# Optimization experiments

Hardware: AMD Instinct MI355X
Metric: run time of the kernel (lower is better)

The kernel has to match this reference:

```python
import jax, jax.numpy as jnp
import numpy as np
from jax import lax

IC = 256
NK = [512, 256, 128]
PS = 16.0  # patch_size
EPS = 1e-5


def conv3x3(x, w, b):
    y = lax.conv_general_dilated(x, w, (1, 1), ((1, 1), (1, 1)),
                                 dimension_numbers=('NCHW', 'OIHW', 'NCHW'))
    return y + b[None, :, None, None]


def conv1x1(x, w, b):
    y = lax.conv_general_dilated(x, w, (1, 1), ((0, 0), (0, 0)),
                                 dimension_numbers=('NCHW', 'OIHW', 'NCHW'))
    return y + b[None, :, None, None]


def bn_eval(x, g, b, m, v):
    inv = lax.rsqrt(v + EPS)
    return (x - m[None, :, None, None]) * (g * inv)[None, :, None, None] + b[None, :, None, None]


def tower(x, w, b, g, bb, m, v, lvl):
    # conv3x3 -> per-level BN (ModuleListDial) -> ReLU, depth=1
    return jax.nn.relu(bn_eval(conv3x3(x, w, b), g[lvl], bb[lvl], m[lvl], v[lvl]))


def setup_inputs() -> dict:
    key = jax.random.key(0)
    ks = jax.random.split(key, 32)
    d = {
        'feat0': jax.random.normal(ks[0], (4, IC, 128, 128), jnp.float32),
        'feat1': jax.random.normal(ks[1], (4, IC, 64, 64), jnp.float32),
        'feat2': jax.random.normal(ks[2], (4, IC, 32, 32), jnp.float32),
        'target_coords': jax.random.randint(ks[3], (2, 32, 32), 0, 32, jnp.int32),
    }
    ki = 4
    for p in ['share', 'ent', 'pat']:
        d[p + '_w'] = jax.random.normal(ks[ki], (IC, IC, 3, 3), jnp.float32) * 0.02; ki += 1
        d[p + '_b'] = jnp.zeros((IC,), jnp.float32)
        d[p + '_g'] = jnp.ones((3, IC), jnp.float32)
        d[p + '_bb'] = jnp.zeros((3, IC), jnp.float32)
        d[p + '_m'] = jax.random.normal(ks[ki], (3, IC), jnp.float32) * 0.1; ki += 1
        d[p + '_v'] = jax.random.uniform(ks[ki], (3, IC), jnp.float32, 0.5, 1.5); ki += 1
    d['ehead_w'] = jax.random.normal(ks[ki], (1, IC, 1, 1), jnp.float32) * 0.05; ki += 1
    d['ehead_b'] = jnp.zeros((1,), jnp.float32)
    d['head_w'] = jax.random.normal(ks[ki], (4, IC), jnp.float32) * 0.05; ki += 1
    d['head_b'] = jnp.zeros((4,), jnp.float32)
    return d


def reference(feat0, feat1, feat2, target_coords,
              share_w, share_b, share_g, share_bb, share_m, share_v,
              ent_w, ent_b, ent_g, ent_bb, ent_m, ent_v,
              pat_w, pat_b, pat_g, pat_bb, pat_m, pat_v,
              ehead_w, ehead_b, head_w, head_b):
    coords = target_coords  # [2, h', w'] (row, col)
    cflat = coords.reshape(2, -1).T  # [P, 2]
    outs = []
    for lvl, (x, nk) in enumerate(zip([feat0, feat1, feat2], NK)):
        xs = tower(x, share_w, share_b, share_g, share_bb, share_m, share_v, lvl)
        ex = tower(xs, ent_w, ent_b, ent_g, ent_bb, ent_m, ent_v, lvl)
        em = jax.nn.sigmoid(conv1x1(ex, ehead_w, ehead_b))  # [B,1,H,W]
        B, C, H, W = ex.shape
        # entropy at candidate anchor points -> [B, P]
        ape = em[:, 0, coords[0], coords[1]].reshape(B, -1)
        _, top_idx = lax.top_k(ape, nk)  # [B, nk]
        xy = cflat[top_idx]  # [B, nk, 2]
        lin = xy[..., 0] * W + xy[..., 1]  # linear index into HW
        px = tower(xs, pat_w, pat_b, pat_g, pat_bb, pat_m, pat_v, lvl)
        pxf = px.reshape(B, C, H * W).transpose(0, 2, 1)  # [B, HW, C]
        af = jnp.take_along_axis(pxf, lin[..., None], axis=1)  # [B, nk, C]
        pc = jax.nn.sigmoid(af @ head_w.T + head_b)  # [B, nk, 4]
        ax = xy[..., 0].astype(pc.dtype)
        ay = xy[..., 1].astype(pc.dtype)
        final = jnp.stack([ax - PS * pc[..., 0], ay - PS * pc[..., 1],
                           ax + PS * pc[..., 2], ay + PS * pc[..., 3]], axis=-1)
        outs += [em, final, xy]
    return tuple(outs)
```

## Files before the change

kernel.cpp:

```cpp
#include <hip/hip_runtime.h>
#include <cstdint>
#include <cstddef>


typedef _Float16 f16;
typedef _Float16 f16x4 __attribute__((ext_vector_type(4)));
typedef _Float16 f16x8 __attribute__((ext_vector_type(8)));
typedef float    f32x4 __attribute__((ext_vector_type(4)));

constexpr int C_CH = 256;
constexpr int KTOT = 2304;
constexpr int PAT_POS = 3584;
constexpr int PAT_N   = PAT_POS * C_CH;

#define GLL16(g, l) __builtin_amdgcn_global_load_lds(                        \
    (const __attribute__((address_space(1))) unsigned int*)(g),              \
    (__attribute__((address_space(3))) unsigned int*)(l), 16, 0, 0)

__global__ __launch_bounds__(256)
void prep_weights_kernel(const float* __restrict__ sw, const float* __restrict__ ew,
                         const float* __restrict__ pw,
                         f16* __restrict__ wTs, f16* __restrict__ wTe,
                         f16* __restrict__ wTsL, f16* __restrict__ wTeL,
                         f16* __restrict__ wTp, f16* __restrict__ wTpL, int n)
{
    int i = blockIdx.x * 256 + threadIdx.x;
    if (i >= n) return;
    const int oc = i / KTOT;
    const int kp = i - oc * KTOT;
    const int tap = kp >> 8;
    const int ic  = kp & 255;
    const int src = oc * KTOT + ic * 9 + tap;
    const float vs = sw[src];
    const f16 hs = (f16)vs;
    wTs[i]  = hs;
    wTsL[i] = (f16)((vs - (float)hs) * 1024.f);
    const float ve = ew[src];
    const f16 he = (f16)ve;
    wTe[i]  = he;
    wTeL[i] = (f16)((ve - (float)he) * 1024.f);
    const float vp = pw[src];
    const f16 hp = (f16)vp;
    wTp[i]  = hp;
    wTpL[i] = (f16)((vp - (float)hp) * 1024.f);
}

__global__ __launch_bounds__(256)
void prep_bn_kernel(const float* sg, const float* sbb, const float* smm,
                    const float* svv, const float* sb,
                    const float* eg, const float* ebb, const float* emm,
                    const float* evv, const float* eb,
                    float* __restrict__ scale, float* __restrict__ shift)
{
    int i = blockIdx.x * 256 + threadIdx.x;
    if (i >= 1536) return;
    const int tw = i / 768;
    const int r  = i - tw * 768;
    const int oc = r & 255;
    float g, bbv, m, v, cb;
    if (tw == 0) { g = sg[r]; bbv = sbb[r]; m = smm[r]; v = svv[r]; cb = sb[oc]; }
    else         { g = eg[r]; bbv = ebb[r]; m = emm[r]; v = evv[r]; cb = eb[oc]; }
    const float inv = 1.0f / sqrtf(v + 1e-5f);
    const float sc = g * inv;
    scale[i] = sc;
    shift[i] = (cb - m) * sc + bbv;
}

__global__ __launch_bounds__(256)
void zero16_kernel(f16x8* __restrict__ p, int n8)
{
    const int i = blockIdx.x * 256 + threadIdx.x;
    if (i < n8) p[i] = (f16x8){};
}

__global__ __launch_bounds__(256)
void fpad16_fill_kernel(const float* __restrict__ feat0,
                        const float* __restrict__ feat1,
                        const float* __restrict__ feat2,
                        f16* __restrict__ xH, f16* __restrict__ xL)
{
    const int h    = blockIdx.x;
    const int lvlb = blockIdx.y;
    const int lvl  = lvlb >> 2, b = lvlb & 3;
    const int logW = 7 - lvl, H = 128 >> lvl;
    if (h >= H) return;
    const int Wv = (H >= 34) ? 34 : 32;
    const int tid = threadIdx.x;
    const float* f = (lvl == 0) ? feat0 : (lvl == 1 ? feat1 : feat2);

    __shared__ float T[34][257];

    const int wl = tid & 31;
    const int cg = tid >> 5;
#pragma unroll
    for (int cb = 0; cb < 32; cb++) {
        const int c = cb * 8 + cg;
        const float* row = f + (((size_t)(b * C_CH + c)) << (2 * logW))
                             + ((size_t)h << logW);
        T[wl][c] = row[wl];
        if (wl < 2 && (wl + 32) < Wv) T[wl + 32][c] = row[wl + 32];
    }
    __syncthreads();
    const size_t rb = ((size_t)lvlb * 1296 + (size_t)(h + 2) * 36 + 2) * 256 + tid;
    for (int w = 0; w < Wv; w++) {
        const float v = T[w][tid];
        const f16 hh = (f16)v;
        xH[rb + (size_t)w * 256] = hh;
        xL[rb + (size_t)w * 256] = (f16)((v - (float)hh) * 1024.f);
    }
}

__global__ __launch_bounds__(256)
void pad_hwc_kernel(const float* __restrict__ feat, f16* __restrict__ xT,
                    int H, int logW)
{
    const int W = 1 << logW;
    const int HW = H << logW;
    const int WP = W + 2, HP = H + 2;
    const int tid = threadIdx.x;
    const int nt  = HW >> 6;
    const int b   = blockIdx.x / nt;
    const int p0  = (blockIdx.x - b * nt) * 64;

    __shared__ f16 T[64][264];

    const int cBase = tid >> 4;
    const int pl4   = (tid & 15) * 4;
#pragma unroll
    for (int it = 0; it < 16; it++) {
        const int c = it * 16 + cBase;
        const float4 v = *(const float4*)(feat + (size_t)(b * C_CH + c) * HW + p0 + pl4);
        T[pl4 + 0][c] = (f16)v.x;
        T[pl4 + 1][c] = (f16)v.y;
        T[pl4 + 2][c] = (f16)v.z;
        T[pl4 + 3][c] = (f16)v.w;
    }
    __syncthreads();
    const int pl = tid >> 2;
    const int c0 = (tid & 3) * 64;
    const int p  = p0 + pl;
    const int h  = p >> logW, w = p & (W - 1);
    f16* dst = xT + ((size_t)(b * HP + h + 1) * WP + (w + 1)) * C_CH + c0;
#pragma unroll
    for (int i = 0; i < 64; i += 8)
        *(f16x8*)(dst + i) = *(const f16x8*)&T[pl][c0 + i];
}

__global__ __launch_bounds__(256)
void zero_cl_border_kernel(f16* __restrict__ xT, int H, int W, int n)
{
    const int WP = W + 2, HP = H + 2;
    const int BS = 2 * WP + 2 * H;
    int i = blockIdx.x * 256 + threadIdx.x;
    if (i >= n) return;
    const int ch = (i & 7) * 32;
    const int bc = i >> 3;
    const int b  = bc / BS;
    const int e  = bc - b * BS;
    int padpos;
    if (e < WP)            padpos = e;
    else if (e < 2 * WP)   padpos = (H + 1) * WP + (e - WP);
    else {
        const int e2 = e - 2 * WP;
        padpos = ((e2 >> 1) + 1) * WP + ((e2 & 1) ? (W + 1) : 0);
    }
    f16* dst = xT + ((size_t)b * HP * WP + padpos) * C_CH + ch;
    const f16x8 z = {};
#pragma unroll
    for (int j = 0; j < 32; j += 8) *(f16x8*)(dst + j) = z;
}

__global__ __launch_bounds__(256, 3)
void conv_mfma_kernel(const f16* __restrict__ xT, const f16* __restrict__ wT,
                      const float* __restrict__ scale,
                      const float* __restrict__ shift,
                      f16* __restrict__ y, int H, int logW, int opad)
{
    const int W  = 1 << logW;
    const int WP = W + 2, HP = H + 2;
    const int HW = H << logW;
    const int tid  = threadIdx.x;
    const int wv   = tid >> 6, lane = tid & 63;

    const int nwg = gridDim.x;
    const int bid = blockIdx.x;
    const int wg  = (bid & 7) * (nwg >> 3) + (bid >> 3);
    const int ocBase = (wg & 1) * 128;
    const int pBase  = (wg >> 1) * 128;
    const int b    = pBase / HW;
    const int rem0 = pBase - b * HW;

    __shared__ f16 sbuf[16384];

    f32x4 acc[4][4];
#pragma unroll
    for (int i = 0; i < 4; i++)
#pragma unroll
        for (int j = 0; j < 4; j++) acc[i][j] = (f32x4){0.f, 0.f, 0.f, 0.f};

    const int lr = lane >> 2, ls = lane & 3;
    const int r0 = (wv * 2) * 16 + lr;
    const int r1 = (wv * 2 + 1) * 16 + lr;
    const int c0s = (ls ^ ((r0 >> 1) & 3)) * 8;
    const int c1s = (ls ^ ((r1 >> 1) & 3)) * 8;
    const f16* aSrc0 = wT + (size_t)(ocBase + r0) * KTOT + c0s;
    const f16* aSrc1 = wT + (size_t)(ocBase + r1) * KTOT + c1s;
    const int pp0 = rem0 + r0, pp1 = rem0 + r1;
    const f16* bSrc0 = xT + ((size_t)(b * HP + (pp0 >> logW) + 1) * WP
                             + (pp0 & (W - 1)) + 1) * C_CH + c0s;
    const f16* bSrc1 = xT + ((size_t)(b * HP + (pp1 >> logW) + 1) * WP
                             + (pp1 & (W - 1)) + 1) * C_CH + c1s;

    const int rw = (wv & 1) * 64;
    const int cw = (wv >> 1) * 64;
    const int lm = lane & 15, lq = lane >> 4;
    int aOff[4], bOff[4];
#pragma unroll
    for (int mi = 0; mi < 4; mi++) {
        const int R = rw + mi * 16 + lm;
        aOff[mi] = R * 32 + ((lq ^ ((R >> 1) & 3)) << 3);
    }
#pragma unroll
    for (int ni = 0; ni < 4; ni++) {
        const int R = cw + ni * 16 + lm;
        bOff[ni] = 4096 + R * 32 + ((lq ^ ((R >> 1) & 3)) << 3);
    }

    auto STAGE = [&](int kn, int nb) {
        const int tap = kn >> 8;
        const int kh  = tap / 3;
        const int kw  = tap - 3 * kh;
        const int tOff = ((kh - 1) * WP + (kw - 1)) * C_CH + (kn & 255);
        f16* lb = &sbuf[nb * 8192 + wv * 1024];
        GLL16(aSrc0 + kn, lb);
        GLL16(aSrc1 + kn, lb + 512);
        GLL16(bSrc0 + tOff, lb + 4096);
        GLL16(bSrc1 + tOff, lb + 4096 + 512);
    };

    STAGE(0, 0);
    __syncthreads();
    int cur = 0;
    for (int k0 = 0; k0 < KTOT; k0 += 32) {
        if (k0 + 32 < KTOT) STAGE(k0 + 32, cur ^ 1);
        const f16* sb = &sbuf[cur * 8192];
        f16x8 af[4], bf[4];
#pragma unroll
        for (int mi = 0; mi < 4; mi++) af[mi] = *(const f16x8*)(sb + aOff[mi]);
#pragma unroll
        for (int ni = 0; ni < 4; ni++) bf[ni] = *(const f16x8*)(sb + bOff[ni]);
#pragma unroll
        for (int mi = 0; mi < 4; mi++)
#pragma unroll
            for (int ni = 0; ni < 4; ni++)
                acc[mi][ni] = __builtin_amdgcn_mfma_f32_16x16x32_f16(
                    af[mi], bf[ni], acc[mi][ni], 0, 0, 0);
        __syncthreads();
        cur ^= 1;
    }

    float sc[4][4], sh[4][4];
#pragma unroll
    for (int mi = 0; mi < 4; mi++)
#pragma unroll
        for (int r = 0; r < 4; r++) {
            const int oc = ocBase + rw + mi * 16 + lq * 4 + r;
            sc[mi][r] = scale[oc];
            sh[mi][r] = shift[oc];
        }
#pragma unroll
    for (int ni = 0; ni < 4; ni++) {
        const int pp = rem0 + cw + ni * 16 + lm;
        size_t dst;
        if (opad) {
            const int h2 = pp >> logW, w2 = pp & (W - 1);
            dst = ((size_t)(b * HP + h2 + 1) * WP + (w2 + 1)) * C_CH;
        } else {
            dst = (size_t)(pBase + cw + ni * 16 + lm) * C_CH;
        }
#pragma unroll
        for (int mi = 0; mi < 4; mi++) {
            const int ocb = ocBase + rw + mi * 16 + lq * 4;
            f16x4 o;
#pragma unroll
            for (int r = 0; r < 4; r++)
                o[r] = (f16)fmaxf(fmaf(acc[mi][ni][r], sc[mi][r], sh[mi][r]), 0.f);
            *(f16x4*)(y + dst + ocb) = o;
        }
    }
}

__global__ __launch_bounds__(256)
void ehead_em_f16_kernel(const f16* __restrict__ ex, const float* __restrict__ ehw,
                         const float* __restrict__ ehb, float* __restrict__ em)
{
    const int wv   = threadIdx.x >> 6;
    const int lane = threadIdx.x & 63;
    const int posBase = (blockIdx.x * 4 + wv) * 8;
    const int sp = lane >> 3;
    const int t  = lane & 7;
    const int cg = t * 32;
    const f16* base = ex + (size_t)(posBase + sp) * C_CH + cg;
    float s = 0.f;
#pragma unroll
    for (int i = 0; i < 32; i += 8) {
        const f16x8 v = *(const f16x8*)(base + i);
#pragma unroll
        for (int j = 0; j < 8; j++)
            s = fmaf((float)v[j], ehw[cg + i + j], s);
    }
    s += __shfl_xor(s, 1);
    s += __shfl_xor(s, 2);
    s += __shfl_xor(s, 4);
    if (t == 0) em[posBase + sp] = 1.0f / (1.0f + expf(-(s + ehb[0])));
}

template<bool IS_SHARE>
__global__ __launch_bounds__(256, 2)
void exact_full_kernel(const f16* __restrict__ xHg, const f16* __restrict__ xLg,
                       const f16* __restrict__ wH, const f16* __restrict__ wL,
                       const float* __restrict__ scale,
                       const float* __restrict__ shift,
                       float* __restrict__ xsp,
                       f16* __restrict__ xOH, f16* __restrict__ xOL,
                       float* __restrict__ apePart, const float* __restrict__ ehw)
{
    constexpr int NTL    = IS_SHARE ? 19 : 16;
    constexpr int IPITCH = IS_SHARE ? 36 : 34;
    constexpr int IPLANE = IS_SHARE ? 1296 : 1156;

    const int tid  = threadIdx.x;
    const int wv   = tid >> 6, lane = tid & 63;

    const int nwg = gridDim.x;
    const int bid = blockIdx.x;
    const int wgs = (bid & 7) * (nwg >> 3) + (bid >> 3);
    const int ocq = wgs & 3;
    const int ti  = wgs >> 2;
    const int lvlb = ti / NTL;
    const int tile = ti - lvlb * NTL;
    const int posBase = tile * 64;
    const int ocBase  = ocq * 64;
    const int lvl  = lvlb >> 2;

    __shared__ f16 sbuf[16384];

    f32x4 accH[2][2], accX[2][2];
#pragma unroll
    for (int i = 0; i < 2; i++)
#pragma unroll
        for (int j = 0; j < 2; j++) {
            accH[i][j] = (f32x4){0.f, 0.f, 0.f, 0.f};
            accX[i][j] = (f32x4){0.f, 0.f, 0.f, 0.f};
        }

    const int lr = lane >> 2, ls = lane & 3;
    const int rA = wv * 16 + lr;
    const int cAs = (ls ^ ((rA >> 1) & 3)) * 8;
    const f16* aSrcH = wH + (size_t)(ocBase + rA) * KTOT + cAs;
    const f16* aSrcL = wL + (size_t)(ocBase + rA) * KTOT + cAs;

    int n = posBase + rA;
    if (IS_SHARE && n > 1155) n = 1155;
    int po;
    if (IS_SHARE) { const int ph = n / 34; po = ph * 36 + (n - ph * 34); }
    else          { po = (n >> 5) * 34 + (n & 31); }
    const f16* bSrcH = xHg + ((size_t)lvlb * IPLANE + po) * 256 + cAs;
    const f16* bSrcL = xLg + ((size_t)lvlb * IPLANE + po) * 256 + cAs;

    const int rw = (wv & 1) * 32;
    const int cw = (wv >> 1) * 32;
    const int lm = lane & 15, lq = lane >> 4;
    int aOff[2], bOff[2];
#pragma unroll
    for (int mi = 0; mi < 2; mi++) {
        const int R = rw + mi * 16 + lm;
        aOff[mi] = R * 32 + ((lq ^ ((R >> 1) & 3)) << 3);
    }
#pragma unroll
    for (int ni = 0; ni < 2; ni++) {
        const int R = cw + ni * 16 + lm;
        bOff[ni] = R * 32 + ((lq ^ ((R >> 1) & 3)) << 3);
    }

    auto STAGE = [&](int kn, int nb) {
        const int tap = kn >> 8;
        const int th  = tap / 3;
        const int tOff = (th * IPITCH + (tap - 3 * th)) * 256 + (kn & 255);
        f16* lb = &sbuf[nb * 8192 + wv * 512];
        GLL16(aSrcH + kn, lb);
        GLL16(aSrcL + kn, lb + 2048);
        GLL16(bSrcH + tOff, lb + 4096);
        GLL16(bSrcL + tOff, lb + 6144);
    };

    STAGE(0, 0);
    __syncthreads();
    int cur = 0;
    for (int ko = 0; ko < KTOT; ko += 32) {
        if (ko + 32 < KTOT) STAGE(ko + 32, cur ^ 1);
        const f16* sb = &sbuf[cur * 8192];
        f16x8 aH[2], aL[2];
#pragma unroll
        for (int mi = 0; mi < 2; mi++) {
            aH[mi] = *(const f16x8*)(sb + aOff[mi]);
            aL[mi] = *(const f16x8*)(sb + 2048 + aOff[mi]);
        }
#pragma unroll
        for (int ni = 0; ni < 2; ni++) {
            const f16x8 bh = *(const f16x8*)(sb + 4096 + bOff[ni]);
            const f16x8 bl = *(const f16x8*)(sb + 6144 + bOff[ni]);
#pragma unroll
            for (int mi = 0; mi < 2; mi++)
                accH[mi][ni] = __builtin_amdgcn_mfma_f32_16x16x32_f16(
                    aH[mi], bh, accH[mi][ni], 0, 0, 0);
#pragma unroll
            for (int mi = 0; mi < 2; mi++)
                accX[mi][ni] = __builtin_amdgcn_mfma_f32_16x16x32_f16(
                    aH[mi], bl, accX[mi][ni], 0, 0, 0);
#pragma unroll
            for (int mi = 0; mi < 2; mi++)
                accX[mi][ni] = __builtin_amdgcn_mfma_f32_16x16x32_f16(
                    aL[mi], bh, accX[mi][ni], 0, 0, 0);
        }
        __syncthreads();
        cur ^= 1;
    }

    if constexpr (IS_SHARE) {
#pragma unroll
        for (int mi = 0; mi < 2; mi++)
#pragma unroll
            for (int r = 0; r < 4; r++) {
                const int chl = rw + mi * 16 + lq * 4 + r;
                const int oc  = ocBase + chl;
                const float sc = scale[lvl * 256 + oc];
                const float sh = shift[lvl * 256 + oc];
#pragma unroll
                for (int ni = 0; ni < 2; ni++) {
                    const int pl  = cw + ni * 16 + lm;
                    const int nn  = posBase + pl;
                    const float val = accH[mi][ni][r]
                                    + accX[mi][ni][r] * (1.0f / 1024.0f);
                    const int ph = nn / 34;
                    const int pw = nn - ph * 34;
                    const bool valid = (nn < 1156) && (ph >= 1) && (pw >= 1) &&
                                       (lvl < 2 || (ph <= 32 && pw <= 32));
                    const float o = valid ? fmaxf(fmaf(val, sc, sh), 0.f) : 0.f;
                    if (nn < 1156)
                        xsp[((size_t)(lvlb * 256 + oc)) * 1156 + nn] = o;
                    const f16 h = (f16)o;
                    sbuf[pl * 72 + chl]        = h;
                    sbuf[4608 + pl * 72 + chl] = (f16)((o - (float)h) * 1024.f);
                }
            }
        __syncthreads();
        const int p  = tid >> 2;
        const int cg = (tid & 3) * 16;
        const int n2 = posBase + p;
        if (n2 < 1156) {
            const size_t gb = ((size_t)lvlb * 1156 + n2) * 256 + ocBase + cg;
            *(f16x8*)(xOH + gb)     = *(const f16x8*)(sbuf + p * 72 + cg);
            *(f16x8*)(xOH + gb + 8) = *(const f16x8*)(sbuf + p * 72 + cg + 8);
            *(f16x8*)(xOL + gb)     = *(const f16x8*)(sbuf + 4608 + p * 72 + cg);
            *(f16x8*)(xOL + gb + 8) = *(const f16x8*)(sbuf + 4608 + p * 72 + cg + 8);
        }
    } else {
        float* pa = (float*)sbuf;
        float pni[2] = {0.f, 0.f};
#pragma unroll
        for (int mi = 0; mi < 2; mi++)
#pragma unroll
            for (int r = 0; r < 4; r++) {
                const int oc = ocBase + rw + mi * 16 + lq * 4 + r;
                const float sc = scale[768 + lvl * 256 + oc];
                const float sh = shift[768 + lvl * 256 + oc];
                const float w  = ehw[oc];
#pragma unroll
                for (int ni = 0; ni < 2; ni++) {
                    const float val = accH[mi][ni][r]
                                    + accX[mi][ni][r] * (1.0f / 1024.0f);
                    pni[ni] = fmaf(w, fmaxf(fmaf(val, sc, sh), 0.f), pni[ni]);
                }
            }
        const int slot = lq + 4 * (wv & 1);
#pragma unroll
        for (int ni = 0; ni < 2; ni++)
            pa[(cw + ni * 16 + lm) * 8 + slot] = pni[ni];
        __syncthreads();
        if (tid < 64) {
            float s = pa[tid * 8];
#pragma unroll
            for (int j = 1; j < 8; j++) s += pa[tid * 8 + j];
            apePart[(size_t)ocq * 12288 + lvlb * 1024 + posBase + tid] = s;
        }
    }
}

__global__ __launch_bounds__(256)
void ape_fin_kernel(const float* __restrict__ apePart,
                    const float* __restrict__ ehb, float* __restrict__ ape)
{
    const int i = blockIdx.x * 256 + threadIdx.x;
    if (i >= 12288) return;
    float s = apePart[i];
    s += apePart[12288 + i];
    s += apePart[24576 + i];
    s += apePart[36864 + i];
    ape[i] = 1.0f / (1.0f + expf(-(s + ehb[0])));
}

__global__ __launch_bounds__(1024)
void topk_all_kernel(const float* __restrict__ ape, const int* __restrict__ coords,
                     int* __restrict__ xy_int, float* __restrict__ out,
                     int xo0, int xo1, int xo2)
{
    const int lvl = blockIdx.x >> 2;
    const int b   = blockIdx.x & 3;
    const int nk  = 512 >> lvl;
    const int tid = threadIdx.x;
    __shared__ unsigned long long keys[1024];

    const int rr = coords[tid] & 31;
    const int cc0 = coords[1024 + tid] & 31;
    const float v = ape[lvl * 4096 + (b << 10) + (rr << 5) + cc0];
    unsigned u = __float_as_uint(v);
    unsigned mono = (u & 0x80000000u) ? ~u : (u | 0x80000000u);
    keys[tid] = (((unsigned long long)(~mono)) << 32) | (unsigned)tid;
    __syncthreads();

    for (int k = 2; k <= 1024; k <<= 1) {
        for (int j = k >> 1; j > 0; j >>= 1) {
            const int ixj = tid ^ j;
            if (ixj > tid) {
                const bool up = ((tid & k) == 0);
                const unsigned long long a = keys[tid], c = keys[ixj];
                if ((a > c) == up) { keys[tid] = c; keys[ixj] = a; }
            }
            __syncthreads();
        }
    }

    if (tid < nk) {
        const int i  = (int)(keys[tid] & 0x3FFu);
        const int r  = coords[i] & 31;
        const int c  = coords[1024 + i] & 31;
        const int intOff = 8192 - (8192 >> lvl);
        const int o  = intOff + (b * nk + tid) * 2;
        xy_int[o]     = r;
        xy_int[o + 1] = c;
        const int xo = (lvl == 0) ? xo0 : (lvl == 1 ? xo1 : xo2);
        out[xo + (b * nk + tid) * 2]     = (float)r;
        out[xo + (b * nk + tid) * 2 + 1] = (float)c;
    }
}

__global__ __launch_bounds__(256, 2)
void pat_mfma_kernel(const f16* __restrict__ xHg, const f16* __restrict__ xLg,
                     const f16* __restrict__ wH, const f16* __restrict__ wL,
                     const int* __restrict__ xy_int,
                     float* __restrict__ part)
{
    const int tid = threadIdx.x;
    const int wv  = tid >> 6, lane = tid & 63;
    const int nwg = gridDim.x;
    const int bid = blockIdx.x;
    const int wgs = (bid & 7) * (nwg >> 3) + (bid >> 3);
    const int z   = wgs & 1;
    const int ocq = (wgs >> 1) & 3;
    const int ti  = wgs >> 3;
    int lvl, pL;
    if (ti < 64)      { lvl = 0; pL = ti * 32; }
    else if (ti < 96) { lvl = 1; pL = (ti - 64) * 32; }
    else              { lvl = 2; pL = (ti - 96) * 32; }
    const int nk   = 512 >> lvl;
    const int bb   = pL / nk;
    const int lvlb = lvl * 4 + bb;
    const int intOff   = 8192 - (8192 >> lvl);
    const int posStart = 4096 - (4096 >> lvl);
    const int ocBase = ocq * 64;
    const int kStart = z * 1152;

    __shared__ f16 sbuf[12288];
    __shared__ int pofs[32];

    if (tid < 32) {
        const int n = pL + tid;
        const int r = xy_int[intOff + n * 2]     & 31;
        const int c = xy_int[intOff + n * 2 + 1] & 31;
        pofs[tid] = r * 34 + c;
    }
    __syncthreads();

    f32x4 accH[2], accX[2];
#pragma unroll
    for (int i = 0; i < 2; i++) {
        accH[i] = (f32x4){0.f, 0.f, 0.f, 0.f};
        accX[i] = (f32x4){0.f, 0.f, 0.f, 0.f};
    }

    const int lr = lane >> 2, ls = lane & 3;
    const int rA  = wv * 16 + lr;
    const int cAs = (ls ^ ((rA >> 1) & 3)) * 8;
    const f16* aSrcH = wH + (size_t)(ocBase + rA) * KTOT + kStart + cAs;
    const f16* aSrcL = wL + (size_t)(ocBase + rA) * KTOT + kStart + cAs;
    const int rB  = (wv & 1) * 16 + lr;
    const int cBs = (ls ^ ((rB >> 1) & 3)) * 8;
    const f16* bBase = (wv < 2) ? xHg : xLg;
    const f16* bSrc = bBase + ((size_t)lvlb * 1156 + pofs[rB]) * 256 + cBs;
    const int bDst = ((wv < 2) ? 4096 : 5120) + (wv & 1) * 512;

    const int rw = (wv & 1) * 32;
    const int pw = (wv >> 1) * 16;
    const int lm = lane & 15, lq = lane >> 4;
    int aOff[2];
#pragma unroll
    for (int mi = 0; mi < 2; mi++) {
        const int R = rw + mi * 16 + lm;
        aOff[mi] = R * 32 + ((lq ^ ((R >> 1) & 3)) << 3);
    }
    const int Rb = pw + lm;
    const int bOff = 4096 + Rb * 32 + ((lq ^ ((Rb >> 1) & 3)) << 3);

    auto STAGE = [&](int kRel, int nb) {
        const int kAbs = kStart + kRel;
        const int tap  = kAbs >> 8;
        const int th   = tap / 3;
        const int tOff = (th * 34 + (tap - 3 * th)) * 256 + (kAbs & 255);
        f16* base = &sbuf[nb * 6144];
        GLL16(aSrcH + kRel, base + wv * 512);
        GLL16(aSrcL + kRel, base + 2048 + wv * 512);
        GLL16(bSrc + tOff,  base + bDst);
    };

    STAGE(0, 0);
    __syncthreads();
    int cur = 0;
    for (int ko = 0; ko < 1152; ko += 32) {
        if (ko + 32 < 1152) STAGE(ko + 32, cur ^ 1);
        const f16* sb = &sbuf[cur * 6144];
        f16x8 aH[2], aL[2];
#pragma unroll
        for (int mi = 0; mi < 2; mi++) {
            aH[mi] = *(const f16x8*)(sb + aOff[mi]);
            aL[mi] = *(const f16x8*)(sb + 2048 + aOff[mi]);
        }
        const f16x8 bh = *(const f16x8*)(sb + bOff);
        const f16x8 bl = *(const f16x8*)(sb + 1024 + bOff);
#pragma unroll
        for (int mi = 0; mi < 2; mi++)
            accH[mi] = __builtin_amdgcn_mfma_f32_16x16x32_f16(
                aH[mi], bh, accH[mi], 0, 0, 0);
#pragma unroll
        for (int mi = 0; mi < 2; mi++)
            accX[mi] = __builtin_amdgcn_mfma_f32_16x16x32_f16(
                aH[mi], bl, accX[mi], 0, 0, 0);
#pragma unroll
        for (int mi = 0; mi < 2; mi++)
            accX[mi] = __builtin_amdgcn_mfma_f32_16x16x32_f16(
                aL[mi], bh, accX[mi], 0, 0, 0);
        __syncthreads();
        cur ^= 1;
    }

    float* op = part + (size_t)z * PAT_N
              + (size_t)(posStart + pL + pw + lm) * C_CH + ocBase;
#pragma unroll
    for (int mi = 0; mi < 2; mi++)
#pragma unroll
        for (int r = 0; r < 4; r++)
            op[rw + mi * 16 + lq * 4 + r] =
                accH[mi][r] + accX[mi][r] * (1.0f / 1024.0f);
}

__global__ __launch_bounds__(256)
void pat_reduce_kernel(const float* __restrict__ part,
                       const float* __restrict__ cb,
                       const float* __restrict__ bng, const float* __restrict__ bnb,
                       const float* __restrict__ bnm, const float* __restrict__ bnv,
                       float* __restrict__ af)
{
    const int i4 = (blockIdx.x * 256 + threadIdx.x) * 4;
    if (i4 >= PAT_N) return;
    const int pos = i4 >> 8;
    const int oc0 = i4 & 255;
    const int lvl = (pos < 2048) ? 0 : (pos < 3072 ? 1 : 2);
    float4 s = *(const float4*)(part + i4);
    {
        const float4 t = *(const float4*)(part + (size_t)PAT_N + i4);
        s.x += t.x; s.y += t.y; s.z += t.z; s.w += t.w;
    }
    const float4 g  = *(const float4*)(bng + lvl * 256 + oc0);
    const float4 bb = *(const float4*)(bnb + lvl * 256 + oc0);
    const float4 m  = *(const float4*)(bnm + lvl * 256 + oc0);
    const float4 v  = *(const float4*)(bnv + lvl * 256 + oc0);
    const float4 cb4 = *(const float4*)(cb + oc0);
    float4 o;
    {
        float inv = 1.0f / sqrtf(v.x + 1e-5f); float sc = g.x * inv;
        o.x = fmaxf(fmaf(s.x, sc, (cb4.x - m.x) * sc + bb.x), 0.f);
        inv = 1.0f / sqrtf(v.y + 1e-5f); sc = g.y * inv;
        o.y = fmaxf(fmaf(s.y, sc, (cb4.y - m.y) * sc + bb.y), 0.f);
        inv = 1.0f / sqrtf(v.z + 1e-5f); sc = g.z * inv;
        o.z = fmaxf(fmaf(s.z, sc, (cb4.z - m.z) * sc + bb.z), 0.f);
        inv = 1.0f / sqrtf(v.w + 1e-5f); sc = g.w * inv;
        o.w = fmaxf(fmaf(s.w, sc, (cb4.w - m.w) * sc + bb.w), 0.f);
    }
    *(float4*)(af + i4) = o;
}

__global__ __launch_bounds__(256)
void head_final_all_kernel(const float* __restrict__ af, const float* __restrict__ hw,
                           const float* __restrict__ hb, const int* __restrict__ xy_int,
                           float* __restrict__ out, int fo0, int fo1, int fo2)
{
    const int pos = blockIdx.x;
    const int lvl = (pos < 2048) ? 0 : (pos < 3072 ? 1 : 2);
    const int local = pos - (4096 - (4096 >> lvl));
    const int intOff = 8192 - (8192 >> lvl);
    const int fo = (lvl == 0) ? fo0 : (lvl == 1 ? fo1 : fo2);
    const int tid  = threadIdx.x;
    const int j4   = tid >> 6;
    const int lane = tid & 63;
    const float* a = af + (size_t)pos * C_CH;
    const float* w = hw + j4 * C_CH;
    float sum = 0.f;
#pragma unroll
    for (int i = 0; i < 4; i++)
        sum = fmaf(a[lane + 64 * i], w[lane + 64 * i], sum);
#pragma unroll
    for (int off = 32; off > 0; off >>= 1) sum += __shfl_down(sum, off);
    if (lane == 0) {
        const float pc = 1.0f / (1.0f + expf(-(sum + hb[j4])));
        const float ax = (float)xy_int[intOff + local * 2];
        const float ay = (float)xy_int[intOff + local * 2 + 1];
        float val;
        if      (j4 == 0) val = ax - 16.0f * pc;
        else if (j4 == 1) val = ay - 16.0f * pc;
        else if (j4 == 2) val = ax + 16.0f * pc;
        else              val = ay + 16.0f * pc;
        out[fo + local * 4 + j4] = val;
    }
}

extern "C" void kernel_launch(void* const* d_in, const int* in_sizes, int n_in,
                              void* d_out, int out_size, void* d_ws, size_t ws_size,
                              hipStream_t stream) {
    const float* feat[3] = {(const float*)d_in[0], (const float*)d_in[1],
                            (const float*)d_in[2]};
    const int*   coords  = (const int*)d_in[3];
    const float* sw  = (const float*)d_in[4];
    const float* sb  = (const float*)d_in[5];
    const float* sg  = (const float*)d_in[6];
    const float* sbb = (const float*)d_in[7];
    const float* smm = (const float*)d_in[8];
    const float* svv = (const float*)d_in[9];
    const float* ew  = (const float*)d_in[10];
    const float* eb  = (const float*)d_in[11];
    const float* eg  = (const float*)d_in[12];
    const float* ebb = (const float*)d_in[13];
    const float* emm = (const float*)d_in[14];
    const float* evv = (const float*)d_in[15];
    const float* pw  = (const float*)d_in[16];
    const float* pb  = (const float*)d_in[17];
    const float* pg  = (const float*)d_in[18];
    const float* pbb = (const float*)d_in[19];
    const float* pmm = (const float*)d_in[20];
    const float* pvv = (const float*)d_in[21];
    const float* ehw = (const float*)d_in[22];
    const float* ehb = (const float*)d_in[23];
    const float* hww = (const float*)d_in[24];
    const float* hbb = (const float*)d_in[25];

    float* out = (float*)d_out;
    char*  ws  = (char*)d_ws;

    f16*   wTs    = (f16*)(ws);
    f16*   wTe    = (f16*)(ws + 1310720);
    f16*   wTsL   = (f16*)(ws + 2621440);
    f16*   wTeL   = (f16*)(ws + 3932160);
    float* scales = (float*)(ws + 5242880);
    float* shifts = (float*)(ws + 5251072);
    f16*   fpadH  = (f16*)(ws + 6291456);
    f16*   fpadL  = (f16*)(ws + 14254080);
    float* patPart= (float*)(ws + 6291456);
    float* af     = (float*)(ws + 23068672);
    f16*   wTp    = (f16*)(ws + 27262976);
    f16*   wTpL   = (f16*)(ws + 28573696);
    f16*   xspH   = (f16*)(ws + 90177536);
    f16*   xspL   = (f16*)(ws + 97280000);
    float* xsp    = (float*)(ws + 104857600);
    float* ape    = (float*)(ws + 119537664);
    int*   xy_int = (int*)  (ws + 119603200);
    float* apePart= (float*)(ws + 119668736);
    f16*   featT  = (f16*)(ws + 27262976);
    f16*   xsT    = (f16*)(ws + 65011712);
    f16*   exT    = (f16*)(ws + 27262976);

    const int Hs[3]    = {128, 64, 32};
    const int logWs[3] = {7, 6, 5};
    const int nks[3]   = {512, 256, 128};

    size_t off = 0;
    size_t emOff[3], finOff[3], xyOff[3];
    for (int l = 0; l < 3; l++) {
        const int HW = Hs[l] * Hs[l];
        emOff[l]  = off; off += (size_t)4 * HW;
        finOff[l] = off; off += (size_t)4 * nks[l] * 4;
        xyOff[l]  = off; off += (size_t)4 * nks[l] * 2;
    }

    prep_weights_kernel<<<(C_CH * KTOT + 255) / 256, 256, 0, stream>>>(
        sw, ew, pw, wTs, wTe, wTsL, wTeL, wTp, wTpL, C_CH * KTOT);
    prep_bn_kernel<<<6, 256, 0, stream>>>(sg, sbb, smm, svv, sb,
                                          eg, ebb, emm, evv, eb, scales, shifts);

    zero16_kernel<<<(995328 + 255) / 256, 256, 0, stream>>>((f16x8*)fpadH, 995328);
    fpad16_fill_kernel<<<dim3(34, 12), 256, 0, stream>>>(
        feat[0], feat[1], feat[2], fpadH, fpadL);
    exact_full_kernel<true><<<912, 256, 0, stream>>>(
        fpadH, fpadL, wTs, wTsL, scales, shifts, xsp, xspH, xspL,
        nullptr, nullptr);
    exact_full_kernel<false><<<768, 256, 0, stream>>>(
        xspH, xspL, wTe, wTeL, scales, shifts, nullptr, nullptr, nullptr,
        apePart, ehw);
    ape_fin_kernel<<<48, 256, 0, stream>>>(apePart, ehb, ape);
    topk_all_kernel<<<12, 1024, 0, stream>>>(
        ape, coords, xy_int, out, (int)xyOff[0], (int)xyOff[1], (int)xyOff[2]);
    pat_mfma_kernel<<<896, 256, 0, stream>>>(
        xspH, xspL, wTp, wTpL, xy_int, patPart);
    pat_reduce_kernel<<<(PAT_N / 1024), 256, 0, stream>>>(
        patPart, pb, pg, pbb, pmm, pvv, af);
    head_final_all_kernel<<<PAT_POS, 256, 0, stream>>>(
        af, hww, hbb, xy_int, out, (int)finOff[0], (int)finOff[1], (int)finOff[2]);

    for (int lvl = 0; lvl < 3; lvl++) {
        const int H = Hs[lvl], logW = logWs[lvl];
        const int W = H;
        const int HW = H << logW;
        const int WP = W + 2;
        const int nbord = 4 * (2 * WP + 2 * H) * 8;

        pad_hwc_kernel<<<4 * HW / 64, 256, 0, stream>>>(feat[lvl], featT, H, logW);
        zero_cl_border_kernel<<<(nbord + 255) / 256, 256, 0, stream>>>(
            featT, H, W, nbord);
        zero_cl_border_kernel<<<(nbord + 255) / 256, 256, 0, stream>>>(
            xsT, H, W, nbord);
        dim3 gconv((4 * HW / 128) * 2);
        conv_mfma_kernel<<<gconv, 256, 0, stream>>>(
            featT, wTs, scales + lvl * 256, shifts + lvl * 256, xsT, H, logW, 1);
        conv_mfma_kernel<<<gconv, 256, 0, stream>>>(
            xsT, wTe, scales + 768 + lvl * 256, shifts + 768 + lvl * 256,
            exT, H, logW, 0);
        ehead_em_f16_kernel<<<4 * HW / 32, 256, 0, stream>>>(
            exT, ehw, ehb, out + emOff[lvl]);
    }
}
```

Baseline: 797.5 us.

## Fuse entropy head into ent conv epilogue and reuse exact level-2 ape

```diff
diff --git a/kernel.cpp b/kernel.cpp
--- a/kernel.cpp
+++ b/kernel.cpp
@@ -174,7 +174,8 @@
 void conv_mfma_kernel(const f16* __restrict__ xT, const f16* __restrict__ wT,
                       const float* __restrict__ scale,
                       const float* __restrict__ shift,
-                      f16* __restrict__ y, int H, int logW, int opad)
+                      f16* __restrict__ y, int H, int logW, int opad,
+                      float* __restrict__ emp, const float* __restrict__ ehw)
 {
     const int W  = 1 << logW;
     const int WP = W + 2, HP = H + 2;
@@ -268,6 +269,36 @@
             sc[mi][r] = scale[oc];
             sh[mi][r] = shift[oc];
         }
+
+    if (emp) {
+        float pni[4] = {0.f, 0.f, 0.f, 0.f};
+#pragma unroll
+        for (int mi = 0; mi < 4; mi++)
+#pragma unroll
+            for (int r = 0; r < 4; r++) {
+                const float w = ehw[ocBase + rw + mi * 16 + lq * 4 + r];
+#pragma unroll
+                for (int ni = 0; ni < 4; ni++) {
+                    const float v = fmaxf(
+                        fmaf(acc[mi][ni][r], sc[mi][r], sh[mi][r]), 0.f);
+                    pni[ni] = fmaf(w, v, pni[ni]);
+                }
+            }
+        float* pa = (float*)sbuf;
+        const int slot = lq + 4 * (wv & 1);
+#pragma unroll
+        for (int ni = 0; ni < 4; ni++)
+            pa[(cw + ni * 16 + lm) * 8 + slot] = pni[ni];
+        __syncthreads();
+        if (tid < 128) {
+            float s = pa[tid * 8];
+#pragma unroll
+            for (int j = 1; j < 8; j++) s += pa[tid * 8 + j];
+            emp[(size_t)(ocBase >> 7) * (4 * (size_t)HW) + pBase + tid] = s;
+        }
+        return;
+    }
+
 #pragma unroll
     for (int ni = 0; ni < 4; ni++) {
         const int pp = rem0 + cw + ni * 16 + lm;
@@ -291,28 +322,20 @@
 }
 
 __global__ __launch_bounds__(256)
-void ehead_em_f16_kernel(const f16* __restrict__ ex, const float* __restrict__ ehw,
-                         const float* __restrict__ ehb, float* __restrict__ em)
-{
-    const int wv   = threadIdx.x >> 6;
-    const int lane = threadIdx.x & 63;
-    const int posBase = (blockIdx.x * 4 + wv) * 8;
-    const int sp = lane >> 3;
-    const int t  = lane & 7;
-    const int cg = t * 32;
-    const f16* base = ex + (size_t)(posBase + sp) * C_CH + cg;
-    float s = 0.f;
-#pragma unroll
-    for (int i = 0; i < 32; i += 8) {
-        const f16x8 v = *(const f16x8*)(base + i);
-#pragma unroll
-        for (int j = 0; j < 8; j++)
-            s = fmaf((float)v[j], ehw[cg + i + j], s);
-    }
-    s += __shfl_xor(s, 1);
-    s += __shfl_xor(s, 2);
-    s += __shfl_xor(s, 4);
-    if (t == 0) em[posBase + sp] = 1.0f / (1.0f + expf(-(s + ehb[0])));
+void em_fin_kernel(const float* __restrict__ emp, const float* __restrict__ ehb,
+                   float* __restrict__ em, int n)
+{
+    const int i = blockIdx.x * 256 + threadIdx.x;
+    if (i >= n) return;
+    const float s = emp[i] + emp[(size_t)n + i] + ehb[0];
+    em[i] = 1.0f / (1.0f + expf(-s));
+}
+
+__global__ __launch_bounds__(256)
+void em2_copy_kernel(const float* __restrict__ ape, float* __restrict__ em)
+{
+    const int i = blockIdx.x * 256 + threadIdx.x;
+    em[i] = ape[8192 + i];
 }
 
 template<bool IS_SHARE>
@@ -321,7 +344,6 @@
                        const f16* __restrict__ wH, const f16* __restrict__ wL,
                        const float* __restrict__ scale,
                        const float* __restrict__ shift,
-                       float* __restrict__ xsp,
                        f16* __restrict__ xOH, f16* __restrict__ xOL,
                        float* __restrict__ apePart, const float* __restrict__ ehw)
 {
@@ -447,8 +469,6 @@
                     const bool valid = (nn < 1156) && (ph >= 1) && (pw >= 1) &&
                                        (lvl < 2 || (ph <= 32 && pw <= 32));
                     const float o = valid ? fmaxf(fmaf(val, sc, sh), 0.f) : 0.f;
-                    if (nn < 1156)
-                        xsp[((size_t)(lvlb * 256 + oc)) * 1156 + nn] = o;
                     const f16 h = (f16)o;
                     sbuf[pl * 72 + chl]        = h;
                     sbuf[4608 + pl * 72 + chl] = (f16)((o - (float)h) * 1024.f);
@@ -784,18 +804,17 @@
     f16*   fpadH  = (f16*)(ws + 6291456);
     f16*   fpadL  = (f16*)(ws + 14254080);
     float* patPart= (float*)(ws + 6291456);
+    float* emPart = (float*)(ws + 6291456);
     float* af     = (float*)(ws + 23068672);
     f16*   wTp    = (f16*)(ws + 27262976);
     f16*   wTpL   = (f16*)(ws + 28573696);
     f16*   xspH   = (f16*)(ws + 90177536);
     f16*   xspL   = (f16*)(ws + 97280000);
-    float* xsp    = (float*)(ws + 104857600);
     float* ape    = (float*)(ws + 119537664);
     int*   xy_int = (int*)  (ws + 119603200);
     float* apePart= (float*)(ws + 119668736);
     f16*   featT  = (f16*)(ws + 27262976);
     f16*   xsT    = (f16*)(ws + 65011712);
-    f16*   exT    = (f16*)(ws + 27262976);
 
     const int Hs[3]    = {128, 64, 32};
     const int logWs[3] = {7, 6, 5};
@@ -819,10 +838,10 @@
     fpad16_fill_kernel<<<dim3(34, 12), 256, 0, stream>>>(
         feat[0], feat[1], feat[2], fpadH, fpadL);
     exact_full_kernel<true><<<912, 256, 0, stream>>>(
-        fpadH, fpadL, wTs, wTsL, scales, shifts, xsp, xspH, xspL,
+        fpadH, fpadL, wTs, wTsL, scales, shifts, xspH, xspL,
         nullptr, nullptr);
     exact_full_kernel<false><<<768, 256, 0, stream>>>(
-        xspH, xspL, wTe, wTeL, scales, shifts, nullptr, nullptr, nullptr,
+        xspH, xspL, wTe, wTeL, scales, shifts, nullptr, nullptr,
         apePart, ehw);
     ape_fin_kernel<<<48, 256, 0, stream>>>(apePart, ehb, ape);
     topk_all_kernel<<<12, 1024, 0, stream>>>(
@@ -834,7 +853,7 @@
     head_final_all_kernel<<<PAT_POS, 256, 0, stream>>>(
         af, hww, hbb, xy_int, out, (int)finOff[0], (int)finOff[1], (int)finOff[2]);
 
-    for (int lvl = 0; lvl < 3; lvl++) {
+    for (int lvl = 0; lvl < 2; lvl++) {
         const int H = Hs[lvl], logW = logWs[lvl];
         const int W = H;
         const int HW = H << logW;
@@ -848,11 +867,13 @@
             xsT, H, W, nbord);
         dim3 gconv((4 * HW / 128) * 2);
         conv_mfma_kernel<<<gconv, 256, 0, stream>>>(
-            featT, wTs, scales + lvl * 256, shifts + lvl * 256, xsT, H, logW, 1);
+            featT, wTs, scales + lvl * 256, shifts + lvl * 256, xsT, H, logW, 1,
+            nullptr, nullptr);
         conv_mfma_kernel<<<gconv, 256, 0, stream>>>(
             xsT, wTe, scales + 768 + lvl * 256, shifts + 768 + lvl * 256,
-            exT, H, logW, 0);
-        ehead_em_f16_kernel<<<4 * HW / 32, 256, 0, stream>>>(
-            exT, ehw, ehb, out + emOff[lvl]);
-    }
-}
+            nullptr, H, logW, 0, emPart, ehw);
+        em_fin_kernel<<<(4 * HW + 255) / 256, 256, 0, stream>>>(
+            emPart, ehb, out + emOff[lvl], 4 * HW);
+    }
+    em2_copy_kernel<<<16, 256, 0, stream>>>(ape, out + emOff[2]);
+}
```

Result: faster. 682.3 us (-14.4%).
